# Kernel tuning notes

Hardware: AMD Instinct MI355X
Metric: run time of the kernel (lower is better)

## Reference

```python
import jax, jax.numpy as jnp
import numpy as np

B, N, C, H, DEPTH, MLP = 8, 1024, 768, 12, 8, 3072
HD = C // H
SCALE = HD ** -0.5
EPS = 1e-5


def layer_norm(x, g, b):
    mu = jnp.mean(x, -1, keepdims=True)
    var = jnp.mean((x - mu) ** 2, -1, keepdims=True)
    return (x - mu) / jnp.sqrt(var + EPS) * g + b


def setup_inputs() -> dict:
    key = jax.random.key(0)
    ks = jax.random.split(key, 8)
    s = 0.02
    return {
        "x": jax.random.normal(ks[0], (B, N, C), jnp.float32),
        "ln1_g": jnp.ones((DEPTH, C), jnp.float32),
        "ln1_b": jnp.zeros((DEPTH, C), jnp.float32),
        "wqkv": jax.random.normal(ks[1], (DEPTH, C, 3 * C), jnp.float32) * s,
        "wproj": jax.random.normal(ks[2], (DEPTH, C, C), jnp.float32) * s,
        "bproj": jnp.zeros((DEPTH, C), jnp.float32),
        "ln2_g": jnp.ones((DEPTH, C), jnp.float32),
        "ln2_b": jnp.zeros((DEPTH, C), jnp.float32),
        "w1": jax.random.normal(ks[3], (DEPTH, C, MLP), jnp.float32) * s,
        "b1": jnp.zeros((DEPTH, MLP), jnp.float32),
        "w2": jax.random.normal(ks[4], (DEPTH, MLP, C), jnp.float32) * s,
        "b2": jnp.zeros((DEPTH, C), jnp.float32),
    }


def reference(x, ln1_g, ln1_b, wqkv, wproj, bproj, ln2_g, ln2_b, w1, b1, w2, b2):
    def body(h, p):
        g1, be1, wq, wp, bp, g2, be2, wf1, bf1, wf2, bf2 = p
        # --- attention block: Residual(PreNorm(SelfAttention)) ---
        y = layer_norm(h, g1, be1)
        qkv = (y @ wq).reshape(B, N, 3, H, HD)
        qkv = jnp.transpose(qkv, (2, 0, 3, 1, 4))  # [3, B, H, N, HD]
        q, k, v = qkv[0], qkv[1], qkv[2]
        logits = jnp.einsum("bhnd,bhmd->bhnm", q, k) * SCALE
        # source applies softmax twice (faithful to original)
        attn = jax.nn.softmax(jax.nn.softmax(logits, axis=-1), axis=-1)
        o = jnp.einsum("bhnm,bhmd->bhnd", attn, v)
        o = jnp.transpose(o, (0, 2, 1, 3)).reshape(B, N, C)
        h = h + o @ wp + bp
        # --- FFN block: Residual(PreNorm(FeedForward)) ---
        y2 = layer_norm(h, g2, be2)
        f = jax.nn.relu(y2 @ wf1 + bf1) @ wf2 + bf2
        return h + f, None

    out, _ = jax.lax.scan(body, x, (ln1_g, ln1_b, wqkv, wproj, bproj, ln2_g, ln2_b, w1, b1, w2, b2))
    return out
```

## Files before the change

### kernel.cpp

```cpp
#include <hip/hip_runtime.h>

#define DEPTHL 8
#define BZ 8
#define SEQ 1024
#define CDIM 768
#define HEADS 12
#define HDIM 64
#define MLPD 3072
#define TOK (BZ*SEQ)
#define QKVN (3*CDIM)

typedef __attribute__((ext_vector_type(8))) short vshort8;
typedef __attribute__((ext_vector_type(4))) short vshort4;
typedef __attribute__((ext_vector_type(4))) float vfloat4;

__device__ __forceinline__ short bf16_bits(float f) {
  union { float f; unsigned u; } x; x.f = f;
  unsigned r = (x.u + 0x7FFFu + ((x.u >> 16) & 1u)) >> 16;
  return (short)r;
}
__device__ __forceinline__ float bits_to_f(short s) {
  union { unsigned u; float f; } x; x.u = ((unsigned)(unsigned short)s) << 16;
  return x.f;
}

#define GL16(g, l) __builtin_amdgcn_global_load_lds( \
    (const __attribute__((address_space(1))) unsigned int*)(g), \
    (__attribute__((address_space(3))) unsigned int*)(l), 16, 0, 0)

__global__ __launch_bounds__(256) void wconv_t(const float* __restrict__ in,
                                               short* __restrict__ out,
                                               int K, int N) {
  __shared__ float tile[32][33];
  const long d = blockIdx.z;
  in  += d * (long)K * N;
  out += d * (long)N * K;
  const int n0 = blockIdx.x * 32, k0 = blockIdx.y * 32;
  const int tx = threadIdx.x & 31, ty = threadIdx.x >> 5;
#pragma unroll
  for (int i = 0; i < 4; i++)
    tile[ty + 8*i][tx] = in[(long)(k0 + ty + 8*i) * N + n0 + tx];
  __syncthreads();
#pragma unroll
  for (int i = 0; i < 4; i++)
    out[(long)(n0 + ty + 8*i) * K + k0 + tx] = bf16_bits(tile[tx][ty + 8*i]);
}

__global__ __launch_bounds__(192) void ln_fwd(const float* __restrict__ h,
                                              const float* __restrict__ g,
                                              const float* __restrict__ be,
                                              short* __restrict__ y) {
  __shared__ float red[3];
  const int row = blockIdx.x;
  const int tid = threadIdx.x;
  const float4 v = ((const float4*)(h + (long)row * CDIM))[tid];
  float s = v.x + v.y + v.z + v.w;
#pragma unroll
  for (int m = 32; m >= 1; m >>= 1) s += __shfl_xor(s, m);
  if ((tid & 63) == 0) red[tid >> 6] = s;
  __syncthreads();
  const float mu = (red[0] + red[1] + red[2]) * (1.0f / CDIM);
  float dx = v.x - mu, dy = v.y - mu, dz = v.z - mu, dw = v.w - mu;
  float q = dx*dx + dy*dy + dz*dz + dw*dw;
  __syncthreads();
#pragma unroll
  for (int m = 32; m >= 1; m >>= 1) q += __shfl_xor(q, m);
  if ((tid & 63) == 0) red[tid >> 6] = q;
  __syncthreads();
  const float rstd = rsqrtf((red[0] + red[1] + red[2]) * (1.0f / CDIM) + 1e-5f);
  const float4 g4 = ((const float4*)g)[tid];
  const float4 b4 = ((const float4*)be)[tid];
  vshort4 o;
  o[0] = bf16_bits(dx * rstd * g4.x + b4.x);
  o[1] = bf16_bits(dy * rstd * g4.y + b4.y);
  o[2] = bf16_bits(dz * rstd * g4.z + b4.z);
  o[3] = bf16_bits(dw * rstd * g4.w + b4.w);
  *(vshort4*)(y + (long)row * CDIM + tid * 4) = o;
}

template<int EPI>
__global__ __launch_bounds__(256) void gemm_bt(const short* __restrict__ A,
                                               const short* __restrict__ Bt,
                                               const float* __restrict__ bias,
                                               void* __restrict__ Cout,
                                               int M, int N, int K) {
  __shared__ short As[128 * 32];
  __shared__ short Bs[128 * 32];
  const int tid = threadIdx.x;
  const int wid = tid >> 6, lane = tid & 63;
  const int lg = lane >> 4, lr = lane & 15;
  const int wm = wid >> 1, wn = wid & 1;
  const long by = blockIdx.y;
  const long bx = blockIdx.x;

  vfloat4 acc[4][4];
#pragma unroll
  for (int i = 0; i < 4; i++)
#pragma unroll
    for (int j = 0; j < 4; j++) acc[i][j] = (vfloat4){0.f, 0.f, 0.f, 0.f};

  const int c = wid * 64 + lane;
  const short* Ag0 = A  + (by * 128 +      (c >> 2)) * (long)K + (c & 3) * 8;
  const short* Ag1 = A  + (by * 128 + 64 + (c >> 2)) * (long)K + (c & 3) * 8;
  const short* Bg0 = Bt + (bx * 128 +      (c >> 2)) * (long)K + (c & 3) * 8;
  const short* Bg1 = Bt + (bx * 128 + 64 + (c >> 2)) * (long)K + (c & 3) * 8;
  short* Al = As + c * 8;
  short* Bl = Bs + c * 8;

  for (int kk = 0; kk < K; kk += 32) {
    __syncthreads();
    GL16(Ag0 + kk, Al);
    GL16(Ag1 + kk, Al + 2048);
    GL16(Bg0 + kk, Bl);
    GL16(Bg1 + kk, Bl + 2048);
    __syncthreads();
    vshort8 a[4], b[4];
#pragma unroll
    for (int mt = 0; mt < 4; mt++)
      a[mt] = *(const vshort8*)(As + (wm * 64 + mt * 16 + lr) * 32 + lg * 8);
#pragma unroll
    for (int nt = 0; nt < 4; nt++)
      b[nt] = *(const vshort8*)(Bs + (wn * 64 + nt * 16 + lr) * 32 + lg * 8);
#pragma unroll
    for (int mt = 0; mt < 4; mt++)
#pragma unroll
      for (int nt = 0; nt < 4; nt++)
        acc[mt][nt] = __builtin_amdgcn_mfma_f32_16x16x32_bf16(a[mt], b[nt], acc[mt][nt], 0, 0, 0);
  }

  const long row0 = by * 128 + wm * 64;
  const long col0 = bx * 128 + wn * 64;
#pragma unroll
  for (int mt = 0; mt < 4; mt++) {
#pragma unroll
    for (int nt = 0; nt < 4; nt++) {
      const long col = col0 + nt * 16 + lr;
      float bv = 0.f;
      if (EPI != 0) bv = bias[col];
#pragma unroll
      for (int r = 0; r < 4; r++) {
        const long row = row0 + mt * 16 + lg * 4 + r;
        float v = acc[mt][nt][r];
        if (EPI == 0) {
          ((short*)Cout)[row * N + col] = bf16_bits(v);
        } else if (EPI == 1) {
          v += bv; v = v > 0.f ? v : 0.f;
          ((short*)Cout)[row * N + col] = bf16_bits(v);
        } else {
          float* hp = (float*)Cout + row * N + col;
          *hp = *hp + v + bv;
        }
      }
    }
  }
}

__global__ __launch_bounds__(256) void attn_fused(const short* __restrict__ qkv,
                                                  short* __restrict__ o) {
  __shared__ short Sb[16 * 1024];
  __shared__ short vT[64 * 72];
  const int qt = blockIdx.x;
  const int bh = blockIdx.y;
  const int b = bh / HEADS, hh = bh % HEADS;
  const int tid = threadIdx.x, wid = tid >> 6, lane = tid & 63;
  const int lg = lane >> 4, lr = lane & 15;
  const long tokbase = (long)b * SEQ;
  const short* qbase = qkv + tokbase * QKVN + hh * HDIM;
  const short* kbase = qbase + CDIM;
  const short* vbase = qbase + 2 * CDIM;

  vshort8 qf[2];
#pragma unroll
  for (int ks = 0; ks < 2; ks++)
    qf[ks] = *(const vshort8*)(qbase + (long)(qt * 16 + lr) * QKVN + ks * 32 + lg * 8);

  for (int i = 0; i < 16; i++) {
    const int n0 = (wid + 4 * i) * 16;
    vfloat4 s = (vfloat4){0.f, 0.f, 0.f, 0.f};
#pragma unroll
    for (int ks = 0; ks < 2; ks++) {
      vshort8 kf = *(const vshort8*)(kbase + (long)(n0 + lr) * QKVN + ks * 32 + lg * 8);
      s = __builtin_amdgcn_mfma_f32_16x16x32_bf16(qf[ks], kf, s, 0, 0, 0);
    }
#pragma unroll
    for (int r = 0; r < 4; r++) {
      const int row = lg * 4 + r;
      const int byt = ((row * 1024 + n0 + lr) * 2) ^ ((row & 7) << 4);
      *(short*)((char*)Sb + byt) = bf16_bits(s[r] * 0.125f);
    }
  }
  __syncthreads();

#pragma unroll
  for (int rr = 0; rr < 4; rr++) {
    const int row = wid * 4 + rr;
    const int base = row * 2048 + lane * 32;
    const int swz = (row & 7) << 4;
    vshort8 e0 = *(const vshort8*)((char*)Sb + (base ^ swz));
    vshort8 e1 = *(const vshort8*)((char*)Sb + ((base + 16) ^ swz));
    float x[16];
#pragma unroll
    for (int j = 0; j < 8; j++) { x[j] = bits_to_f(e0[j]); x[8 + j] = bits_to_f(e1[j]); }
    float m = x[0];
#pragma unroll
    for (int j = 1; j < 16; j++) m = fmaxf(m, x[j]);
#pragma unroll
    for (int sh = 1; sh < 64; sh <<= 1) m = fmaxf(m, __shfl_xor(m, sh));
    float z = 0.f;
#pragma unroll
    for (int j = 0; j < 16; j++) { x[j] = __expf(x[j] - m); z += x[j]; }
#pragma unroll
    for (int sh = 1; sh < 64; sh <<= 1) z += __shfl_xor(z, sh);
    const float rz = 1.0f / z;
    float t2 = 0.f;
#pragma unroll
    for (int j = 0; j < 16; j++) { x[j] = __expf(x[j] * rz); t2 += x[j]; }
#pragma unroll
    for (int sh = 1; sh < 64; sh <<= 1) t2 += __shfl_xor(t2, sh);
    const float rt = 1.0f / t2;
    vshort8 o0, o1;
#pragma unroll
    for (int j = 0; j < 8; j++) { o0[j] = bf16_bits(x[j] * rt); o1[j] = bf16_bits(x[8 + j] * rt); }
    *(vshort8*)((char*)Sb + (base ^ swz)) = o0;
    *(vshort8*)((char*)Sb + ((base + 16) ^ swz)) = o1;
  }

  vfloat4 oacc = (vfloat4){0.f, 0.f, 0.f, 0.f};
  for (int kt = 0; kt < 16; kt++) {
    const int d0 = (tid & 7) * 8;
    const int kvp = (tid >> 3) * 2;
    const short* vr = vbase + (long)(kt * 64 + kvp) * QKVN + d0;
    vshort8 v0 = *(const vshort8*)vr;
    vshort8 v1 = *(const vshort8*)(vr + QKVN);
    __syncthreads();
#pragma unroll
    for (int j = 0; j < 8; j++) {
      unsigned pk = ((unsigned)(unsigned short)v0[j]) | (((unsigned)(unsigned short)v1[j]) << 16);
      *(unsigned*)((char*)vT + ((d0 + j) * 72 + kvp) * 2) = pk;
    }
    __syncthreads();
#pragma unroll
    for (int ks = 0; ks < 2; ks++) {
      const int kv0 = kt * 64 + ks * 32;
      const int abyt = ((lr * 1024 + kv0 + lg * 8) * 2) ^ ((lr & 7) << 4);
      vshort8 af = *(const vshort8*)((char*)Sb + abyt);
      vshort8 bfr = *(const vshort8*)(vT + (wid * 16 + lr) * 72 + ks * 32 + lg * 8);
      oacc = __builtin_amdgcn_mfma_f32_16x16x32_bf16(af, bfr, oacc, 0, 0, 0);
    }
  }

#pragma unroll
  for (int r = 0; r < 4; r++) {
    const long row = tokbase + qt * 16 + lg * 4 + r;
    o[row * CDIM + hh * HDIM + wid * 16 + lr] = bf16_bits(oacc[r]);
  }
}

extern "C" void kernel_launch(void* const* d_in, const int* in_sizes, int n_in,
                              void* d_out, int out_size, void* d_ws, size_t ws_size,
                              hipStream_t stream) {
  const float* x     = (const float*)d_in[0];
  const float* ln1_g = (const float*)d_in[1];
  const float* ln1_b = (const float*)d_in[2];
  const float* wqkv  = (const float*)d_in[3];
  const float* wproj = (const float*)d_in[4];
  const float* bproj = (const float*)d_in[5];
  const float* ln2_g = (const float*)d_in[6];
  const float* ln2_b = (const float*)d_in[7];
  const float* w1    = (const float*)d_in[8];
  const float* b1    = (const float*)d_in[9];
  const float* w2    = (const float*)d_in[10];
  const float* b2    = (const float*)d_in[11];
  float* h = (float*)d_out;

  char* ws = (char*)d_ws;
  short* wqkv_t  = (short*)ws; ws += (size_t)DEPTHL * QKVN * CDIM * 2;
  short* wproj_t = (short*)ws; ws += (size_t)DEPTHL * CDIM * CDIM * 2;
  short* w1_t    = (short*)ws; ws += (size_t)DEPTHL * MLPD * CDIM * 2;
  short* w2_t    = (short*)ws; ws += (size_t)DEPTHL * CDIM * MLPD * 2;
  short* ybf     = (short*)ws; ws += (size_t)TOK * CDIM * 2;
  short* qkvbf   = (short*)ws; ws += (size_t)TOK * QKVN * 2;
  short* obf     = (short*)ws; ws += (size_t)TOK * CDIM * 2;
  short* f1bf    = (short*)ws; ws += (size_t)TOK * MLPD * 2;

  hipMemcpyAsync(h, x, (size_t)TOK * CDIM * sizeof(float), hipMemcpyDeviceToDevice, stream);

  wconv_t<<<dim3(QKVN / 32, CDIM / 32, DEPTHL), 256, 0, stream>>>(wqkv, wqkv_t, CDIM, QKVN);
  wconv_t<<<dim3(CDIM / 32, CDIM / 32, DEPTHL), 256, 0, stream>>>(wproj, wproj_t, CDIM, CDIM);
  wconv_t<<<dim3(MLPD / 32, CDIM / 32, DEPTHL), 256, 0, stream>>>(w1, w1_t, CDIM, MLPD);
  wconv_t<<<dim3(CDIM / 32, MLPD / 32, DEPTHL), 256, 0, stream>>>(w2, w2_t, MLPD, CDIM);

  for (int l = 0; l < DEPTHL; l++) {
    ln_fwd<<<TOK, 192, 0, stream>>>(h, ln1_g + l * CDIM, ln1_b + l * CDIM, ybf);
    gemm_bt<0><<<dim3(QKVN / 128, TOK / 128), 256, 0, stream>>>(
        ybf, wqkv_t + (size_t)l * QKVN * CDIM, nullptr, qkvbf, TOK, QKVN, CDIM);
    attn_fused<<<dim3(SEQ / 16, BZ * HEADS), 256, 0, stream>>>(qkvbf, obf);
    gemm_bt<2><<<dim3(CDIM / 128, TOK / 128), 256, 0, stream>>>(
        obf, wproj_t + (size_t)l * CDIM * CDIM, bproj + l * CDIM, h, TOK, CDIM, CDIM);
    ln_fwd<<<TOK, 192, 0, stream>>>(h, ln2_g + l * CDIM, ln2_b + l * CDIM, ybf);
    gemm_bt<1><<<dim3(MLPD / 128, TOK / 128), 256, 0, stream>>>(
        ybf, w1_t + (size_t)l * MLPD * CDIM, b1 + l * MLPD, f1bf, TOK, MLPD, CDIM);
    gemm_bt<2><<<dim3(CDIM / 128, TOK / 128), 256, 0, stream>>>(
        f1bf, w2_t + (size_t)l * CDIM * MLPD, b2 + l * CDIM, h, TOK, CDIM, MLPD);
  }
}
```

Before: 3.750 ms.

## Keep attention scores in registers and pre-transpose V in a separate kernel

Attention is restructured so the QK^T scores stay in registers as fp32. Softmax max and sums are reduced with cross-lane shuffles plus a small shared-memory exchange, which removes the bf16 round trip of the scores through LDS before the double softmax. V is transposed once per layer by a new vtrans kernel into a scratch buffer that aliases the FFN intermediate buffer. The PV loop then reads V^T fragments straight from global memory, with no per-tile LDS transpose and its two barriers. The cost is one extra kernel launch, an extra pass over V in memory, and higher register pressure from holding 64 score floats per lane.

Result: faster. 3.589 ms (-4.3%).

```diff
diff --git a/kernel.cpp b/kernel.cpp
--- a/kernel.cpp
+++ b/kernel.cpp
@@ -19,10 +19,6 @@
   unsigned r = (x.u + 0x7FFFu + ((x.u >> 16) & 1u)) >> 16;
   return (short)r;
 }
-__device__ __forceinline__ float bits_to_f(short s) {
-  union { unsigned u; float f; } x; x.u = ((unsigned)(unsigned short)s) << 16;
-  return x.f;
-}
 
 #define GL16(g, l) __builtin_amdgcn_global_load_lds( \
     (const __attribute__((address_space(1))) unsigned int*)(g), \
@@ -44,6 +40,24 @@
 #pragma unroll
   for (int i = 0; i < 4; i++)
     out[(long)(n0 + ty + 8*i) * K + k0 + tx] = bf16_bits(tile[tx][ty + 8*i]);
+}
+
+__global__ __launch_bounds__(256) void vtrans(const short* __restrict__ qkv,
+                                              short* __restrict__ vt) {
+  __shared__ short tile[32][34];
+  const int bh = blockIdx.z;
+  const int b = bh / HEADS, hh = bh % HEADS;
+  const int t0 = blockIdx.x * 32, d0 = blockIdx.y * 32;
+  const int tx = threadIdx.x & 31, ty = threadIdx.x >> 5;
+  const short* src = qkv + ((long)b * SEQ + t0) * QKVN + 2 * CDIM + hh * HDIM + d0;
+#pragma unroll
+  for (int i = 0; i < 4; i++)
+    tile[ty + 8*i][tx] = src[(long)(ty + 8*i) * QKVN + tx];
+  __syncthreads();
+  short* dst = vt + (long)bh * HDIM * SEQ + (long)d0 * SEQ + t0;
+#pragma unroll
+  for (int i = 0; i < 4; i++)
+    dst[(long)(ty + 8*i) * SEQ + tx] = tile[tx][ty + 8*i];
 }
 
 __global__ __launch_bounds__(192) void ln_fwd(const float* __restrict__ h,
@@ -155,104 +169,104 @@
   }
 }
 
-__global__ __launch_bounds__(256) void attn_fused(const short* __restrict__ qkv,
-                                                  short* __restrict__ o) {
-  __shared__ short Sb[16 * 1024];
-  __shared__ short vT[64 * 72];
-  const int qt = blockIdx.x;
-  const int bh = blockIdx.y;
+__global__ __launch_bounds__(256) void attn_fused2(const short* __restrict__ qkv,
+                                                   const short* __restrict__ vt,
+                                                   short* __restrict__ o) {
+  __shared__ short P_lds[16 * 1024];
+  __shared__ float redm[4][16], redz[4][16], redt[4][16];
+  const int qt = blockIdx.x, bh = blockIdx.y;
   const int b = bh / HEADS, hh = bh % HEADS;
   const int tid = threadIdx.x, wid = tid >> 6, lane = tid & 63;
   const int lg = lane >> 4, lr = lane & 15;
   const long tokbase = (long)b * SEQ;
   const short* qbase = qkv + tokbase * QKVN + hh * HDIM;
   const short* kbase = qbase + CDIM;
-  const short* vbase = qbase + 2 * CDIM;
+  const short* vtb = vt + (long)bh * HDIM * SEQ;
 
   vshort8 qf[2];
 #pragma unroll
   for (int ks = 0; ks < 2; ks++)
     qf[ks] = *(const vshort8*)(qbase + (long)(qt * 16 + lr) * QKVN + ks * 32 + lg * 8);
 
+  vfloat4 s[16];
+#pragma unroll
   for (int i = 0; i < 16; i++) {
-    const int n0 = (wid + 4 * i) * 16;
-    vfloat4 s = (vfloat4){0.f, 0.f, 0.f, 0.f};
+    const int n0 = wid * 256 + i * 16;
+    vfloat4 acc = (vfloat4){0.f, 0.f, 0.f, 0.f};
 #pragma unroll
     for (int ks = 0; ks < 2; ks++) {
       vshort8 kf = *(const vshort8*)(kbase + (long)(n0 + lr) * QKVN + ks * 32 + lg * 8);
-      s = __builtin_amdgcn_mfma_f32_16x16x32_bf16(qf[ks], kf, s, 0, 0, 0);
+      acc = __builtin_amdgcn_mfma_f32_16x16x32_bf16(kf, qf[ks], acc, 0, 0, 0);
     }
-#pragma unroll
-    for (int r = 0; r < 4; r++) {
-      const int row = lg * 4 + r;
-      const int byt = ((row * 1024 + n0 + lr) * 2) ^ ((row & 7) << 4);
-      *(short*)((char*)Sb + byt) = bf16_bits(s[r] * 0.125f);
-    }
-  }
-  __syncthreads();
-
-#pragma unroll
-  for (int rr = 0; rr < 4; rr++) {
-    const int row = wid * 4 + rr;
-    const int base = row * 2048 + lane * 32;
-    const int swz = (row & 7) << 4;
-    vshort8 e0 = *(const vshort8*)((char*)Sb + (base ^ swz));
-    vshort8 e1 = *(const vshort8*)((char*)Sb + ((base + 16) ^ swz));
-    float x[16];
-#pragma unroll
-    for (int j = 0; j < 8; j++) { x[j] = bits_to_f(e0[j]); x[8 + j] = bits_to_f(e1[j]); }
-    float m = x[0];
-#pragma unroll
-    for (int j = 1; j < 16; j++) m = fmaxf(m, x[j]);
-#pragma unroll
-    for (int sh = 1; sh < 64; sh <<= 1) m = fmaxf(m, __shfl_xor(m, sh));
-    float z = 0.f;
-#pragma unroll
-    for (int j = 0; j < 16; j++) { x[j] = __expf(x[j] - m); z += x[j]; }
-#pragma unroll
-    for (int sh = 1; sh < 64; sh <<= 1) z += __shfl_xor(z, sh);
-    const float rz = 1.0f / z;
-    float t2 = 0.f;
-#pragma unroll
-    for (int j = 0; j < 16; j++) { x[j] = __expf(x[j] * rz); t2 += x[j]; }
-#pragma unroll
-    for (int sh = 1; sh < 64; sh <<= 1) t2 += __shfl_xor(t2, sh);
-    const float rt = 1.0f / t2;
-    vshort8 o0, o1;
-#pragma unroll
-    for (int j = 0; j < 8; j++) { o0[j] = bf16_bits(x[j] * rt); o1[j] = bf16_bits(x[8 + j] * rt); }
-    *(vshort8*)((char*)Sb + (base ^ swz)) = o0;
-    *(vshort8*)((char*)Sb + ((base + 16) ^ swz)) = o1;
-  }
-
+    s[i][0] = acc[0] * 0.125f; s[i][1] = acc[1] * 0.125f;
+    s[i][2] = acc[2] * 0.125f; s[i][3] = acc[3] * 0.125f;
+  }
+
+  vfloat4 mv = s[0];
+#pragma unroll
+  for (int i = 1; i < 16; i++) {
+    mv[0] = fmaxf(mv[0], s[i][0]); mv[1] = fmaxf(mv[1], s[i][1]);
+    mv[2] = fmaxf(mv[2], s[i][2]); mv[3] = fmaxf(mv[3], s[i][3]);
+  }
+  float m = fmaxf(fmaxf(mv[0], mv[1]), fmaxf(mv[2], mv[3]));
+  m = fmaxf(m, __shfl_xor(m, 16));
+  m = fmaxf(m, __shfl_xor(m, 32));
+  if (lane < 16) redm[wid][lr] = m;
+  __syncthreads();
+  m = fmaxf(fmaxf(redm[0][lr], redm[1][lr]), fmaxf(redm[2][lr], redm[3][lr]));
+
+  float z = 0.f;
+#pragma unroll
+  for (int i = 0; i < 16; i++) {
+#pragma unroll
+    for (int r = 0; r < 4; r++) { s[i][r] = __expf(s[i][r] - m); z += s[i][r]; }
+  }
+  z += __shfl_xor(z, 16);
+  z += __shfl_xor(z, 32);
+  if (lane < 16) redz[wid][lr] = z;
+  __syncthreads();
+  z = redz[0][lr] + redz[1][lr] + redz[2][lr] + redz[3][lr];
+  const float rz = 1.0f / z;
+
+  float t2 = 0.f;
+#pragma unroll
+  for (int i = 0; i < 16; i++) {
+#pragma unroll
+    for (int r = 0; r < 4; r++) { s[i][r] = __expf(s[i][r] * rz); t2 += s[i][r]; }
+  }
+  t2 += __shfl_xor(t2, 16);
+  t2 += __shfl_xor(t2, 32);
+  if (lane < 16) redt[wid][lr] = t2;
+  __syncthreads();
+  t2 = redt[0][lr] + redt[1][lr] + redt[2][lr] + redt[3][lr];
+  const float rt = 1.0f / t2;
+
+#pragma unroll
+  for (int i = 0; i < 16; i++) {
+    const int sbase = lr * 1024 + wid * 256 + i * 16 + lg * 4;
+    const int byt = (sbase * 2) ^ ((lr & 7) << 4);
+    vshort4 pk;
+    pk[0] = bf16_bits(s[i][0] * rt); pk[1] = bf16_bits(s[i][1] * rt);
+    pk[2] = bf16_bits(s[i][2] * rt); pk[3] = bf16_bits(s[i][3] * rt);
+    *(vshort4*)((char*)P_lds + byt) = pk;
+  }
+  __syncthreads();
+
+  const int dt = wid;
   vfloat4 oacc = (vfloat4){0.f, 0.f, 0.f, 0.f};
-  for (int kt = 0; kt < 16; kt++) {
-    const int d0 = (tid & 7) * 8;
-    const int kvp = (tid >> 3) * 2;
-    const short* vr = vbase + (long)(kt * 64 + kvp) * QKVN + d0;
-    vshort8 v0 = *(const vshort8*)vr;
-    vshort8 v1 = *(const vshort8*)(vr + QKVN);
-    __syncthreads();
-#pragma unroll
-    for (int j = 0; j < 8; j++) {
-      unsigned pk = ((unsigned)(unsigned short)v0[j]) | (((unsigned)(unsigned short)v1[j]) << 16);
-      *(unsigned*)((char*)vT + ((d0 + j) * 72 + kvp) * 2) = pk;
-    }
-    __syncthreads();
-#pragma unroll
-    for (int ks = 0; ks < 2; ks++) {
-      const int kv0 = kt * 64 + ks * 32;
-      const int abyt = ((lr * 1024 + kv0 + lg * 8) * 2) ^ ((lr & 7) << 4);
-      vshort8 af = *(const vshort8*)((char*)Sb + abyt);
-      vshort8 bfr = *(const vshort8*)(vT + (wid * 16 + lr) * 72 + ks * 32 + lg * 8);
-      oacc = __builtin_amdgcn_mfma_f32_16x16x32_bf16(af, bfr, oacc, 0, 0, 0);
-    }
+  const short* vrow = vtb + (long)(dt * 16 + lr) * SEQ + lg * 8;
+#pragma unroll 8
+  for (int win = 0; win < 32; win++) {
+    const int abyt = (lr * 2048 + win * 64 + lg * 16) ^ ((lr & 7) << 4);
+    vshort8 af = *(const vshort8*)((char*)P_lds + abyt);
+    vshort8 bfr = *(const vshort8*)(vrow + win * 32);
+    oacc = __builtin_amdgcn_mfma_f32_16x16x32_bf16(af, bfr, oacc, 0, 0, 0);
   }
 
 #pragma unroll
   for (int r = 0; r < 4; r++) {
     const long row = tokbase + qt * 16 + lg * 4 + r;
-    o[row * CDIM + hh * HDIM + wid * 16 + lr] = bf16_bits(oacc[r]);
+    o[row * CDIM + hh * HDIM + dt * 16 + lr] = bf16_bits(oacc[r]);
   }
 }
 
@@ -282,6 +296,7 @@
   short* qkvbf   = (short*)ws; ws += (size_t)TOK * QKVN * 2;
   short* obf     = (short*)ws; ws += (size_t)TOK * CDIM * 2;
   short* f1bf    = (short*)ws; ws += (size_t)TOK * MLPD * 2;
+  short* vtb     = f1bf;
 
   hipMemcpyAsync(h, x, (size_t)TOK * CDIM * sizeof(float), hipMemcpyDeviceToDevice, stream);
 
@@ -294,7 +309,8 @@
     ln_fwd<<<TOK, 192, 0, stream>>>(h, ln1_g + l * CDIM, ln1_b + l * CDIM, ybf);
     gemm_bt<0><<<dim3(QKVN / 128, TOK / 128), 256, 0, stream>>>(
         ybf, wqkv_t + (size_t)l * QKVN * CDIM, nullptr, qkvbf, TOK, QKVN, CDIM);
-    attn_fused<<<dim3(SEQ / 16, BZ * HEADS), 256, 0, stream>>>(qkvbf, obf);
+    vtrans<<<dim3(SEQ / 32, HDIM / 32, BZ * HEADS), 256, 0, stream>>>(qkvbf, vtb);
+    attn_fused2<<<dim3(SEQ / 16, BZ * HEADS), 256, 0, stream>>>(qkvbf, vtb, obf);
     gemm_bt<2><<<dim3(CDIM / 128, TOK / 128), 256, 0, stream>>>(
         obf, wproj_t + (size_t)l * CDIM * CDIM, bproj + l * CDIM, h, TOK, CDIM, CDIM);
     ln_fwd<<<TOK, 192, 0, stream>>>(h, ln2_g + l * CDIM, ln2_b + l * CDIM, ybf);
```
